# Kernel tuning notes

Hardware: AMD Instinct MI355X
Metric: run time of the kernel (lower is better)

Reference implementation:

```python
import jax, jax.numpy as jnp
import numpy as np

EPS = 1e-5

def layer_norm(x, gamma, beta):
    mu = jnp.mean(x, axis=-1, keepdims=True)
    var = jnp.mean(jnp.square(x - mu), axis=-1, keepdims=True)
    return (x - mu) * jax.lax.rsqrt(var + EPS) * gamma + beta

def setup_inputs() -> dict:
    key = jax.random.key(0)
    ks = jax.random.split(key, 8)
    B, N, CZ, C = 1, 512, 128, 128
    s_z = 1.0 / np.sqrt(CZ)
    s_c = 1.0 / np.sqrt(C)
    return {
        "pair_rep": jax.random.normal(ks[0], (B, N, N, CZ), dtype=jnp.float32),
        "ln1_gamma": jnp.ones((CZ,), jnp.float32),
        "ln1_beta": jnp.zeros((CZ,), jnp.float32),
        "w_gate_a": jax.random.normal(ks[1], (CZ, C), jnp.float32) * s_z,
        "w_gate_b": jax.random.normal(ks[2], (CZ, C), jnp.float32) * s_z,
        "w_a": jax.random.normal(ks[3], (CZ, C), jnp.float32) * s_z,
        "w_b": jax.random.normal(ks[4], (CZ, C), jnp.float32) * s_z,
        "ln2_gamma": jnp.ones((C,), jnp.float32),
        "ln2_beta": jnp.zeros((C,), jnp.float32),
        "w_out": jax.random.normal(ks[5], (C, CZ), jnp.float32) * s_c,
        "w_gate": jax.random.normal(ks[6], (CZ, CZ), jnp.float32) * s_z,
    }

def reference(pair_rep, ln1_gamma, ln1_beta, w_gate_a, w_gate_b, w_a, w_b,
              ln2_gamma, ln2_beta, w_out, w_gate):
    # pair_rep: [B, N, N, CZ]
    z = layer_norm(pair_rep, ln1_gamma, ln1_beta)
    a = jax.nn.sigmoid(z @ w_gate_a) * (z @ w_a)   # [B, N, N, C]
    b = jax.nn.sigmoid(z @ w_gate_b) * (z @ w_b)   # [B, N, N, C]
    g = jax.nn.sigmoid(z @ w_gate)                 # [B, N, N, CZ]
    # triangle multiplicative update (outgoing): sum over third node k
    upd = jnp.einsum('bikc,bjkc->bijc', a, b)      # [B, N, N, C]
    upd = layer_norm(upd, ln2_gamma, ln2_beta) @ w_out  # [B, N, N, CZ]
    return g * upd
```

## Files before the change

kernel.cpp:

```cpp
#include <hip/hip_runtime.h>

#define N_ 512
#define NPOS (N_*N_)
#define CD 128

typedef unsigned short ushort_t;
typedef unsigned int   uint_t;
typedef __bf16 bf16_t;
typedef bf16_t  bf16x8 __attribute__((ext_vector_type(8)));
typedef float   f32x4  __attribute__((ext_vector_type(4)));
typedef unsigned short u16x4 __attribute__((ext_vector_type(4)));
typedef uint_t  u32x4 __attribute__((ext_vector_type(4)));

__device__ __forceinline__ float bf2f(ushort_t h) {
  union { uint_t u; float f; } v; v.u = ((uint_t)h) << 16; return v.f;
}
__device__ __forceinline__ ushort_t f2bf(float f) {
  union { float f; uint_t u; } v; v.f = f;
  uint_t u = v.u;
  return (ushort_t)((u + 0x7FFFu + ((u >> 16) & 1u)) >> 16);
}
__device__ __forceinline__ float sigm(float x) { return 1.0f / (1.0f + __expf(-x)); }

__global__ void k_tw(const float* s0, const float* s1, const float* s2,
                     const float* s3, const float* s4, const float* s5,
                     ushort_t* dst) {
  const float* s;
  switch (blockIdx.x) {
    case 0: s = s0; break; case 1: s = s1; break; case 2: s = s2; break;
    case 3: s = s3; break; case 4: s = s4; break; default: s = s5; break;
  }
  ushort_t* d = dst + blockIdx.x * CD * CD;
  for (int idx = threadIdx.x; idx < CD * CD; idx += 256) {
    int c = idx >> 7, k = idx & 127;
    d[idx] = f2bf(s[k * CD + c]);
  }
}

__global__ void k_ln1(const float* __restrict__ x, const float* __restrict__ gma,
                      const float* __restrict__ bta, ushort_t* __restrict__ z) {
  const int tid  = threadIdx.x;
  const int l15  = tid & 15;
  const int row  = blockIdx.x * 16 + (tid >> 4);
  const float4* src = (const float4*)(x + (size_t)row * CD + l15 * 8);
  float4 v0 = src[0], v1 = src[1];
  float s = ((v0.x + v0.y) + (v0.z + v0.w)) + ((v1.x + v1.y) + (v1.z + v1.w));
  float q = ((v0.x*v0.x + v0.y*v0.y) + (v0.z*v0.z + v0.w*v0.w))
          + ((v1.x*v1.x + v1.y*v1.y) + (v1.z*v1.z + v1.w*v1.w));
  #pragma unroll
  for (int o = 1; o < 16; o <<= 1) { s += __shfl_xor(s, o, 64); q += __shfl_xor(q, o, 64); }
  float mu = s * (1.0f / 128.0f);
  float rs = rsqrtf(q * (1.0f / 128.0f) - mu * mu + 1e-5f);
  const float4* gp = (const float4*)(gma + l15 * 8);
  const float4* bp = (const float4*)(bta + l15 * 8);
  float4 g0 = gp[0], g1v = gp[1], b0 = bp[0], b1v = bp[1];
  uint_t w0 = (uint_t)f2bf((v0.x-mu)*rs*g0.x +b0.x ) | ((uint_t)f2bf((v0.y-mu)*rs*g0.y +b0.y ) << 16);
  uint_t w1 = (uint_t)f2bf((v0.z-mu)*rs*g0.z +b0.z ) | ((uint_t)f2bf((v0.w-mu)*rs*g0.w +b0.w ) << 16);
  uint_t w2 = (uint_t)f2bf((v1.x-mu)*rs*g1v.x+b1v.x) | ((uint_t)f2bf((v1.y-mu)*rs*g1v.y+b1v.y) << 16);
  uint_t w3 = (uint_t)f2bf((v1.z-mu)*rs*g1v.z+b1v.z) | ((uint_t)f2bf((v1.w-mu)*rs*g1v.w+b1v.w) << 16);
  u32x4 pk = {w0, w1, w2, w3};
  *(u32x4*)(z + (size_t)row * CD + l15 * 8) = pk;
}

__global__ __launch_bounds__(256, 1)
void k_proj(const ushort_t* __restrict__ z, const ushort_t* __restrict__ wT,
            ushort_t* __restrict__ aT, ushort_t* __restrict__ bT) {
  __shared__ ushort_t zl[128 * 128];
  __shared__ ushort_t tb[128][136];
  const int tid = threadIdx.x;
  const int lane = tid & 63, w = tid >> 6;
  const int qd = lane >> 4, l15 = lane & 15;

  bf16x8 wf[4][2][4];
  #pragma unroll
  for (int m = 0; m < 4; ++m)
    #pragma unroll
    for (int i = 0; i < 2; ++i)
      #pragma unroll
      for (int kk = 0; kk < 4; ++kk)
        wf[m][i][kk] = *(const bf16x8*)(wT + m * CD * CD + (w * 32 + i * 16 + l15) * CD + kk * 32 + qd * 8);

  const int TILES = 4;
  const int base = blockIdx.x * TILES;

  u32x4 st[8];
  {
    const u32x4* src = (const u32x4*)(z + (size_t)base * 128 * CD);
    #pragma unroll
    for (int i = 0; i < 8; ++i) st[i] = src[tid + i * 256];
  }

  for (int t = 0; t < TILES; ++t) {
    const int pos0 = (base + t) * 128;
    __syncthreads();
    {
      u32x4* dst = (u32x4*)zl;
      #pragma unroll
      for (int i = 0; i < 8; ++i) {
        int u = tid + i * 256, row = u >> 4;
        dst[(u & ~15) | ((u & 15) ^ (row & 7))] = st[i];
      }
    }
    __syncthreads();
    if (t + 1 < TILES) {
      const u32x4* src = (const u32x4*)(z + (size_t)(base + t + 1) * 128 * CD);
      #pragma unroll
      for (int i = 0; i < 8; ++i) st[i] = src[tid + i * 256];
    }

    #pragma unroll
    for (int ab = 0; ab < 2; ++ab) {
      f32x4 ag[2][8] = {}; f32x4 av[2][8] = {};
      #pragma unroll
      for (int kk = 0; kk < 4; ++kk) {
        bf16x8 zf[8];
        #pragma unroll
        for (int j = 0; j < 8; ++j) {
          int row = j * 16 + l15, kq = kk * 4 + qd;
          zf[j] = ((const bf16x8*)zl)[(row << 4) | (kq ^ (row & 7))];
        }
        #pragma unroll
        for (int j = 0; j < 8; ++j)
          #pragma unroll
          for (int i = 0; i < 2; ++i) {
            ag[i][j] = __builtin_amdgcn_mfma_f32_16x16x32_bf16(wf[ab * 2][i][kk],     zf[j], ag[i][j], 0, 0, 0);
            av[i][j] = __builtin_amdgcn_mfma_f32_16x16x32_bf16(wf[ab * 2 + 1][i][kk], zf[j], av[i][j], 0, 0, 0);
          }
      }
      #pragma unroll
      for (int i = 0; i < 2; ++i)
        #pragma unroll
        for (int j = 0; j < 8; ++j)
          #pragma unroll
          for (int r = 0; r < 4; ++r)
            tb[w * 32 + i * 16 + qd * 4 + r][j * 16 + l15] = f2bf(sigm(ag[i][j][r]) * av[i][j][r]);
      __syncthreads();
      {
        ushort_t* dst = ab ? bT : aT;
        #pragma unroll
        for (int it = 0; it < 8; ++it) {
          int idx = tid + it * 256;
          int row = idx >> 4, c16 = idx & 15;
          u32x4 v = *(const u32x4*)&tb[row][c16 * 8];
          *(u32x4*)&dst[(size_t)row * NPOS + pos0 + c16 * 8] = v;
        }
      }
      __syncthreads();
    }
  }
}

__device__ __forceinline__ int uofs(int row, int c4) {
  return (row * 4 + (c4 ^ ((row >> 1) & 3))) * 8;
}
__global__ void k_tri(const ushort_t* __restrict__ aT, const ushort_t* __restrict__ bT,
                      ushort_t* __restrict__ uT) {
  __shared__ u32x4 smem4[2176];
  ushort_t* lds = (ushort_t*)smem4;
  const int tid = threadIdx.x;
  const int lane = tid & 63, wid = tid >> 6;
  const int qd = lane >> 4, l15 = lane & 15;
  const int wm = wid & 1, wn = wid >> 1;
  const int c  = blockIdx.z;
  const int m0 = blockIdx.y * 128, n0 = blockIdx.x * 128;
  const ushort_t* A = aT + (size_t)c * NPOS;
  const ushort_t* B = bT + (size_t)c * NPOS;
  const int sr = tid >> 2, c4 = tid & 3;

  u32x4 rA0, rA1, rB0, rB1;
  rA0 = *(const u32x4*)&A[(size_t)(m0 + sr)      * N_ + c4 * 8];
  rA1 = *(const u32x4*)&A[(size_t)(m0 + 64 + sr) * N_ + c4 * 8];
  rB0 = *(const u32x4*)&B[(size_t)(n0 + sr)      * N_ + c4 * 8];
  rB1 = *(const u32x4*)&B[(size_t)(n0 + 64 + sr) * N_ + c4 * 8];
  *(u32x4*)&lds[       uofs(sr,      c4)] = rA0;
  *(u32x4*)&lds[       uofs(sr + 64, c4)] = rA1;
  *(u32x4*)&lds[8192 + uofs(sr,      c4)] = rB0;
  *(u32x4*)&lds[8192 + uofs(sr + 64, c4)] = rB1;

  f32x4 acc[4][4] = {};
  for (int it = 1; it <= 16; ++it) {
    __syncthreads();
    const int curb = (it - 1) & 1, nxt = it & 1;
    if (it < 16) {
      const int ko = it * 32;
      rA0 = *(const u32x4*)&A[(size_t)(m0 + sr)      * N_ + ko + c4 * 8];
      rA1 = *(const u32x4*)&A[(size_t)(m0 + 64 + sr) * N_ + ko + c4 * 8];
      rB0 = *(const u32x4*)&B[(size_t)(n0 + sr)      * N_ + ko + c4 * 8];
      rB1 = *(const u32x4*)&B[(size_t)(n0 + 64 + sr) * N_ + ko + c4 * 8];
    }
    const ushort_t* la = lds + curb * 4096;
    const ushort_t* lb = lds + 8192 + curb * 4096;
    bf16x8 af[4], bfr[4];
    #pragma unroll
    for (int t = 0; t < 4; ++t) af[t]  = *(const bf16x8*)&la[uofs(wm * 64 + t * 16 + l15, qd)];
    #pragma unroll
    for (int t = 0; t < 4; ++t) bfr[t] = *(const bf16x8*)&lb[uofs(wn * 64 + t * 16 + l15, qd)];
    #pragma unroll
    for (int i = 0; i < 4; ++i)
      #pragma unroll
      for (int j = 0; j < 4; ++j)
        acc[i][j] = __builtin_amdgcn_mfma_f32_16x16x32_bf16(af[i], bfr[j], acc[i][j], 0, 0, 0);
    if (it < 16) {
      *(u32x4*)&lds[nxt * 4096 +        uofs(sr,      c4)] = rA0;
      *(u32x4*)&lds[nxt * 4096 +        uofs(sr + 64, c4)] = rA1;
      *(u32x4*)&lds[8192 + nxt * 4096 + uofs(sr,      c4)] = rB0;
      *(u32x4*)&lds[8192 + nxt * 4096 + uofs(sr + 64, c4)] = rB1;
    }
  }
  __syncthreads();
  ushort_t (*tb)[136] = (ushort_t(*)[136])smem4;
  #pragma unroll
  for (int i = 0; i < 4; ++i)
    #pragma unroll
    for (int j = 0; j < 4; ++j)
      #pragma unroll
      for (int r2 = 0; r2 < 4; ++r2)
        tb[wm * 64 + i * 16 + qd * 4 + r2][wn * 64 + j * 16 + l15] = f2bf(acc[i][j][r2]);
  __syncthreads();
  ushort_t* U = uT + (size_t)c * NPOS;
  #pragma unroll
  for (int it = 0; it < 8; ++it) {
    int idx = tid + it * 256;
    int row = idx >> 4, c16 = idx & 15;
    u32x4 v = *(const u32x4*)&tb[row][c16 * 8];
    *(u32x4*)&U[(size_t)(m0 + row) * N_ + n0 + c16 * 8] = v;
  }
}

__global__ __launch_bounds__(256, 2)
void k_out(const ushort_t* __restrict__ uT, const ushort_t* __restrict__ wT,
           const float* __restrict__ pair,
           const float* __restrict__ g1, const float* __restrict__ b1,
           const float* __restrict__ g2, const float* __restrict__ b2,
           float* __restrict__ gout) {
  __shared__ ushort_t nu[128][136];
  __shared__ ushort_t zn[128][136];
  __shared__ float ps[2][128], pq[2][128];
  __shared__ float mu[128], rsd[128], gam[128], bet[128];
  const int tid = threadIdx.x;
  const int lane = tid & 63, wid = tid >> 6;
  const int qd = lane >> 4, l15 = lane & 15;
  const int pos0 = blockIdx.x * 128;
  const ushort_t* WgT = wT + 4 * CD * CD;
  const ushort_t* WoT = wT + 5 * CD * CD;

  if (tid < 128) { gam[tid] = g2[tid]; bet[tid] = b2[tid]; }

  {
    int r = tid >> 1, h = tid & 1;
    const float4* src = (const float4*)(pair + (size_t)(pos0 + r) * CD + h * 64);
    float s = 0.f, sq = 0.f;
    #pragma unroll
    for (int u = 0; u < 16; ++u) {
      float4 v = src[u];
      s  += (v.x + v.y) + (v.z + v.w);
      sq += (v.x*v.x + v.y*v.y) + (v.z*v.z + v.w*v.w);
    }
    ps[h][r] = s; pq[h][r] = sq;
  }
  __syncthreads();
  if (tid < 128) {
    float s = ps[0][tid] + ps[1][tid];
    float m = s * (1.0f / 128.0f);
    float v = (pq[0][tid] + pq[1][tid]) * (1.0f / 128.0f) - m * m;
    mu[tid] = m; rsd[tid] = rsqrtf(v + 1e-5f);
  }
  __syncthreads();
  {
    int r = tid >> 1, h = tid & 1;
    float m = mu[r], rs = rsd[r];
    const float4* src = (const float4*)(pair + (size_t)(pos0 + r) * CD + h * 64);
    const float4* gp = (const float4*)(g1 + h * 64);
    const float4* bp = (const float4*)(b1 + h * 64);
    #pragma unroll
    for (int u2 = 0; u2 < 8; ++u2) {
      float4 v0 = src[u2*2], v1 = src[u2*2+1];
      float4 ga = gp[u2*2], gb2 = gp[u2*2+1];
      float4 ba = bp[u2*2], bb2 = bp[u2*2+1];
      uint_t w0 = (uint_t)f2bf((v0.x-m)*rs*ga.x +ba.x ) | ((uint_t)f2bf((v0.y-m)*rs*ga.y +ba.y ) << 16);
      uint_t w1 = (uint_t)f2bf((v0.z-m)*rs*ga.z +ba.z ) | ((uint_t)f2bf((v0.w-m)*rs*ga.w +ba.w ) << 16);
      uint_t w2 = (uint_t)f2bf((v1.x-m)*rs*gb2.x+bb2.x) | ((uint_t)f2bf((v1.y-m)*rs*gb2.y+bb2.y) << 16);
      uint_t w3 = (uint_t)f2bf((v1.z-m)*rs*gb2.z+bb2.z) | ((uint_t)f2bf((v1.w-m)*rs*gb2.w+bb2.w) << 16);
      u32x4 pk = {w0, w1, w2, w3};
      *(u32x4*)&zn[r][h * 64 + u2 * 8] = pk;
    }
  }
  __syncthreads();

  {
    int p = tid & 127, h = tid >> 7;
    float s = 0.f, sq = 0.f;
    for (int cc = h * 64; cc < h * 64 + 64; ++cc) {
      ushort_t raw = uT[(size_t)cc * NPOS + pos0 + p];
      nu[p][cc] = raw;
      float v = bf2f(raw); s += v; sq += v * v;
    }
    ps[h][p] = s; pq[h][p] = sq;
  }
  __syncthreads();
  if (tid < 128) {
    float s = ps[0][tid] + ps[1][tid];
    float m = s * (1.0f / 128.0f);
    float v = (pq[0][tid] + pq[1][tid]) * (1.0f / 128.0f) - m * m;
    mu[tid] = m; rsd[tid] = rsqrtf(v + 1e-5f);
  }
  __syncthreads();
  {
    int p = tid & 127, h = tid >> 7;
    float m = mu[p], rs = rsd[p];
    for (int cc = h * 64; cc < h * 64 + 64; ++cc)
      nu[p][cc] = f2bf((bf2f(nu[p][cc]) - m) * rs * gam[cc] + bet[cc]);
  }
  __syncthreads();

  const int wm = wid & 1, wn = wid >> 1;
  f32x4 ao[4][4] = {}; f32x4 agt[4][4] = {};
  for (int kk = 0; kk < 4; ++kk) {
    bf16x8 afo[4], afg[4];
    #pragma unroll
    for (int i = 0; i < 4; ++i) {
      int wrow = (wm * 64 + i * 16 + l15) * CD + kk * 32 + qd * 8;
      afo[i] = *(const bf16x8*)(WoT + wrow);
      afg[i] = *(const bf16x8*)(WgT + wrow);
    }
    #pragma unroll
    for (int j = 0; j < 4; ++j) {
      bf16x8 bn = *(const bf16x8*)&nu[wn * 64 + j * 16 + l15][kk * 32 + qd * 8];
      bf16x8 bz = *(const bf16x8*)&zn[wn * 64 + j * 16 + l15][kk * 32 + qd * 8];
      #pragma unroll
      for (int i = 0; i < 4; ++i) {
        ao[i][j]  = __builtin_amdgcn_mfma_f32_16x16x32_bf16(afo[i], bn, ao[i][j],  0, 0, 0);
        agt[i][j] = __builtin_amdgcn_mfma_f32_16x16x32_bf16(afg[i], bz, agt[i][j], 0, 0, 0);
      }
    }
  }
  #pragma unroll
  for (int i = 0; i < 4; ++i) {
    int cz = wm * 64 + i * 16 + qd * 4;
    #pragma unroll
    for (int j = 0; j < 4; ++j) {
      int pos = pos0 + wn * 64 + j * 16 + l15;
      float4 pk;
      pk.x = sigm(agt[i][j][0]) * ao[i][j][0];
      pk.y = sigm(agt[i][j][1]) * ao[i][j][1];
      pk.z = sigm(agt[i][j][2]) * ao[i][j][2];
      pk.w = sigm(agt[i][j][3]) * ao[i][j][3];
      *(float4*)&gout[(size_t)pos * CD + cz] = pk;
    }
  }
}

extern "C" void kernel_launch(void* const* d_in, const int* in_sizes, int n_in,
                              void* d_out, int out_size, void* d_ws, size_t ws_size,
                              hipStream_t stream) {
  const float* pair = (const float*)d_in[0];
  const float* g1   = (const float*)d_in[1];
  const float* b1   = (const float*)d_in[2];
  const float* wga  = (const float*)d_in[3];
  const float* wgb  = (const float*)d_in[4];
  const float* wa   = (const float*)d_in[5];
  const float* wb   = (const float*)d_in[6];
  const float* g2   = (const float*)d_in[7];
  const float* b2   = (const float*)d_in[8];
  const float* wout = (const float*)d_in[9];
  const float* wg   = (const float*)d_in[10];

  char* ws = (char*)d_ws;
  ushort_t* z  = (ushort_t*)(ws);
  ushort_t* aT = (ushort_t*)(ws + 67108864);
  ushort_t* bT = (ushort_t*)(ws + 134217728);
  ushort_t* wT = (ushort_t*)(ws + 201326592);
  ushort_t* uT = z;
  float*    gb = (float*)d_out;

  k_tw  <<<6, 256, 0, stream>>>(wga, wa, wgb, wb, wg, wout, wT);
  k_ln1 <<<NPOS / 16, 256, 0, stream>>>(pair, g1, b1, z);
  k_proj<<<512, 256, 0, stream>>>(z, wT, aT, bT);
  k_tri <<<dim3(4, 4, 128), 256, 0, stream>>>(aT, bT, uT);
  k_out <<<2048, 256, 0, stream>>>(uT, wT, pair, g1, b1, g2, b2, gb);
}
```

Measured before the change: 547.0 us.

## Move gate projection into k_proj and fold LN2 affine into output weights

```diff
diff --git a/kernel.cpp b/kernel.cpp
--- a/kernel.cpp
+++ b/kernel.cpp
@@ -15,6 +15,12 @@
 __device__ __forceinline__ float bf2f(ushort_t h) {
   union { uint_t u; float f; } v; v.u = ((uint_t)h) << 16; return v.f;
 }
+__device__ __forceinline__ float bf2f_lo(uint_t w) {
+  union { uint_t u; float f; } v; v.u = w << 16; return v.f;
+}
+__device__ __forceinline__ float bf2f_hi(uint_t w) {
+  union { uint_t u; float f; } v; v.u = w & 0xffff0000u; return v.f;
+}
 __device__ __forceinline__ ushort_t f2bf(float f) {
   union { float f; uint_t u; } v; v.f = f;
   uint_t u = v.u;
@@ -24,16 +30,32 @@
 
 __global__ void k_tw(const float* s0, const float* s1, const float* s2,
                      const float* s3, const float* s4, const float* s5,
-                     ushort_t* dst) {
+                     ushort_t* dst, const float* lg2, const float* lb2, float* K12) {
   const float* s;
   switch (blockIdx.x) {
     case 0: s = s0; break; case 1: s = s1; break; case 2: s = s2; break;
     case 3: s = s3; break; case 4: s = s4; break; default: s = s5; break;
   }
   ushort_t* d = dst + blockIdx.x * CD * CD;
-  for (int idx = threadIdx.x; idx < CD * CD; idx += 256) {
-    int c = idx >> 7, k = idx & 127;
-    d[idx] = f2bf(s[k * CD + c]);
+  if (blockIdx.x == 5) {
+    for (int idx = threadIdx.x; idx < CD * CD; idx += 256) {
+      int cz = idx >> 7, ci = idx & 127;
+      d[idx] = f2bf(s[ci * CD + cz] * lg2[ci]);
+    }
+    if (threadIdx.x < 128) {
+      int cz = threadIdx.x;
+      float k1 = 0.f, k2 = 0.f;
+      for (int ci = 0; ci < 128; ++ci) {
+        float w = s[ci * CD + cz];
+        k1 += lg2[ci] * w; k2 += lb2[ci] * w;
+      }
+      K12[cz] = k1; K12[128 + cz] = k2;
+    }
+  } else {
+    for (int idx = threadIdx.x; idx < CD * CD; idx += 256) {
+      int c = idx >> 7, k = idx & 127;
+      d[idx] = f2bf(s[k * CD + c]);
+    }
   }
 }
 
@@ -64,16 +86,17 @@
 
 __global__ __launch_bounds__(256, 1)
 void k_proj(const ushort_t* __restrict__ z, const ushort_t* __restrict__ wT,
-            ushort_t* __restrict__ aT, ushort_t* __restrict__ bT) {
+            ushort_t* __restrict__ aT, ushort_t* __restrict__ bT,
+            float* __restrict__ g) {
   __shared__ ushort_t zl[128 * 128];
   __shared__ ushort_t tb[128][136];
   const int tid = threadIdx.x;
   const int lane = tid & 63, w = tid >> 6;
   const int qd = lane >> 4, l15 = lane & 15;
 
-  bf16x8 wf[4][2][4];
-  #pragma unroll
-  for (int m = 0; m < 4; ++m)
+  bf16x8 wf[5][2][4];
+  #pragma unroll
+  for (int m = 0; m < 5; ++m)
     #pragma unroll
     for (int i = 0; i < 2; ++i)
       #pragma unroll
@@ -146,6 +169,36 @@
         }
       }
       __syncthreads();
+    }
+
+    {
+      f32x4 acc[2][8] = {};
+      #pragma unroll
+      for (int kk = 0; kk < 4; ++kk) {
+        bf16x8 zf[8];
+        #pragma unroll
+        for (int j = 0; j < 8; ++j) {
+          int row = j * 16 + l15, kq = kk * 4 + qd;
+          zf[j] = ((const bf16x8*)zl)[(row << 4) | (kq ^ (row & 7))];
+        }
+        #pragma unroll
+        for (int j = 0; j < 8; ++j)
+          #pragma unroll
+          for (int i = 0; i < 2; ++i)
+            acc[i][j] = __builtin_amdgcn_mfma_f32_16x16x32_bf16(wf[4][i][kk], zf[j], acc[i][j], 0, 0, 0);
+      }
+      #pragma unroll
+      for (int i = 0; i < 2; ++i) {
+        int cz = w * 32 + i * 16 + qd * 4;
+        #pragma unroll
+        for (int j = 0; j < 8; ++j) {
+          int pos = pos0 + j * 16 + l15;
+          float4 pk;
+          pk.x = sigm(acc[i][j][0]); pk.y = sigm(acc[i][j][1]);
+          pk.z = sigm(acc[i][j][2]); pk.w = sigm(acc[i][j][3]);
+          *(float4*)&g[(size_t)pos * CD + cz] = pk;
+        }
+      }
     }
   }
 }
@@ -227,124 +280,105 @@
   }
 }
 
+__device__ __forceinline__ int nuofs(int row, int c16) {
+  return (row * 17 + (c16 ^ ((row >> 3) & 7))) * 8;
+}
 __global__ __launch_bounds__(256, 2)
 void k_out(const ushort_t* __restrict__ uT, const ushort_t* __restrict__ wT,
-           const float* __restrict__ pair,
-           const float* __restrict__ g1, const float* __restrict__ b1,
-           const float* __restrict__ g2, const float* __restrict__ b2,
-           float* __restrict__ gout) {
-  __shared__ ushort_t nu[128][136];
-  __shared__ ushort_t zn[128][136];
-  __shared__ float ps[2][128], pq[2][128];
-  __shared__ float mu[128], rsd[128], gam[128], bet[128];
+           const float* __restrict__ K12, float* gout) {
+  __shared__ ushort_t nu[128 * 17 * 8];
+  __shared__ float red[2][4][16][8];
+  __shared__ float muL[128], rsL[128], K1s[128], K2s[128];
   const int tid = threadIdx.x;
   const int lane = tid & 63, wid = tid >> 6;
   const int qd = lane >> 4, l15 = lane & 15;
   const int pos0 = blockIdx.x * 128;
-  const ushort_t* WgT = wT + 4 * CD * CD;
+  const int pch = tid & 15, cbase = tid >> 4;
   const ushort_t* WoT = wT + 5 * CD * CD;
 
-  if (tid < 128) { gam[tid] = g2[tid]; bet[tid] = b2[tid]; }
-
-  {
-    int r = tid >> 1, h = tid & 1;
-    const float4* src = (const float4*)(pair + (size_t)(pos0 + r) * CD + h * 64);
-    float s = 0.f, sq = 0.f;
-    #pragma unroll
-    for (int u = 0; u < 16; ++u) {
-      float4 v = src[u];
-      s  += (v.x + v.y) + (v.z + v.w);
-      sq += (v.x*v.x + v.y*v.y) + (v.z*v.z + v.w*v.w);
-    }
-    ps[h][r] = s; pq[h][r] = sq;
+  if (tid < 128) { K1s[tid] = K12[tid]; K2s[tid] = K12[128 + tid]; }
+
+  uint_t c8[8][4];
+  #pragma unroll
+  for (int i = 0; i < 8; ++i) {
+    u32x4 v = *(const u32x4*)&uT[(size_t)(cbase * 8 + i) * NPOS + pos0 + pch * 8];
+    c8[i][0] = v[0]; c8[i][1] = v[1]; c8[i][2] = v[2]; c8[i][3] = v[3];
+  }
+
+  float s8[8] = {}, q8[8] = {};
+  #pragma unroll
+  for (int i = 0; i < 8; ++i)
+    #pragma unroll
+    for (int wd = 0; wd < 4; ++wd) {
+      float vlo = bf2f_lo(c8[i][wd]), vhi = bf2f_hi(c8[i][wd]);
+      s8[wd * 2]     += vlo; q8[wd * 2]     += vlo * vlo;
+      s8[wd * 2 + 1] += vhi; q8[wd * 2 + 1] += vhi * vhi;
+    }
+  #pragma unroll
+  for (int r = 0; r < 8; ++r) {
+    s8[r] += __shfl_xor(s8[r], 16, 64); q8[r] += __shfl_xor(q8[r], 16, 64);
+    s8[r] += __shfl_xor(s8[r], 32, 64); q8[r] += __shfl_xor(q8[r], 32, 64);
+  }
+  if (lane < 16) {
+    #pragma unroll
+    for (int r = 0; r < 8; ++r) { red[0][wid][lane][r] = s8[r]; red[1][wid][lane][r] = q8[r]; }
+  }
+
+  #pragma unroll
+  for (int r = 0; r < 8; ++r) {
+    u32x4 t;
+    #pragma unroll
+    for (int k = 0; k < 4; ++k) {
+      uint_t a = c8[2 * k][r >> 1], b = c8[2 * k + 1][r >> 1];
+      uint_t sh = (r & 1) * 16;
+      t[k] = ((a >> sh) & 0xffffu) | (((b >> sh) & 0xffffu) << 16);
+    }
+    *(u32x4*)&nu[nuofs(pch * 8 + r, cbase)] = t;
   }
   __syncthreads();
+
   if (tid < 128) {
-    float s = ps[0][tid] + ps[1][tid];
+    int p2 = tid >> 3, r2 = tid & 7;
+    float s = red[0][0][p2][r2] + red[0][1][p2][r2] + red[0][2][p2][r2] + red[0][3][p2][r2];
+    float q = red[1][0][p2][r2] + red[1][1][p2][r2] + red[1][2][p2][r2] + red[1][3][p2][r2];
     float m = s * (1.0f / 128.0f);
-    float v = (pq[0][tid] + pq[1][tid]) * (1.0f / 128.0f) - m * m;
-    mu[tid] = m; rsd[tid] = rsqrtf(v + 1e-5f);
+    float v = q * (1.0f / 128.0f) - m * m;
+    muL[tid] = m; rsL[tid] = rsqrtf(v + 1e-5f);
   }
   __syncthreads();
-  {
-    int r = tid >> 1, h = tid & 1;
-    float m = mu[r], rs = rsd[r];
-    const float4* src = (const float4*)(pair + (size_t)(pos0 + r) * CD + h * 64);
-    const float4* gp = (const float4*)(g1 + h * 64);
-    const float4* bp = (const float4*)(b1 + h * 64);
-    #pragma unroll
-    for (int u2 = 0; u2 < 8; ++u2) {
-      float4 v0 = src[u2*2], v1 = src[u2*2+1];
-      float4 ga = gp[u2*2], gb2 = gp[u2*2+1];
-      float4 ba = bp[u2*2], bb2 = bp[u2*2+1];
-      uint_t w0 = (uint_t)f2bf((v0.x-m)*rs*ga.x +ba.x ) | ((uint_t)f2bf((v0.y-m)*rs*ga.y +ba.y ) << 16);
-      uint_t w1 = (uint_t)f2bf((v0.z-m)*rs*ga.z +ba.z ) | ((uint_t)f2bf((v0.w-m)*rs*ga.w +ba.w ) << 16);
-      uint_t w2 = (uint_t)f2bf((v1.x-m)*rs*gb2.x+bb2.x) | ((uint_t)f2bf((v1.y-m)*rs*gb2.y+bb2.y) << 16);
-      uint_t w3 = (uint_t)f2bf((v1.z-m)*rs*gb2.z+bb2.z) | ((uint_t)f2bf((v1.w-m)*rs*gb2.w+bb2.w) << 16);
-      u32x4 pk = {w0, w1, w2, w3};
-      *(u32x4*)&zn[r][h * 64 + u2 * 8] = pk;
-    }
-  }
-  __syncthreads();
-
-  {
-    int p = tid & 127, h = tid >> 7;
-    float s = 0.f, sq = 0.f;
-    for (int cc = h * 64; cc < h * 64 + 64; ++cc) {
-      ushort_t raw = uT[(size_t)cc * NPOS + pos0 + p];
-      nu[p][cc] = raw;
-      float v = bf2f(raw); s += v; sq += v * v;
-    }
-    ps[h][p] = s; pq[h][p] = sq;
-  }
-  __syncthreads();
-  if (tid < 128) {
-    float s = ps[0][tid] + ps[1][tid];
-    float m = s * (1.0f / 128.0f);
-    float v = (pq[0][tid] + pq[1][tid]) * (1.0f / 128.0f) - m * m;
-    mu[tid] = m; rsd[tid] = rsqrtf(v + 1e-5f);
-  }
-  __syncthreads();
-  {
-    int p = tid & 127, h = tid >> 7;
-    float m = mu[p], rs = rsd[p];
-    for (int cc = h * 64; cc < h * 64 + 64; ++cc)
-      nu[p][cc] = f2bf((bf2f(nu[p][cc]) - m) * rs * gam[cc] + bet[cc]);
-  }
-  __syncthreads();
 
   const int wm = wid & 1, wn = wid >> 1;
-  f32x4 ao[4][4] = {}; f32x4 agt[4][4] = {};
+  f32x4 acc[4][4] = {};
   for (int kk = 0; kk < 4; ++kk) {
-    bf16x8 afo[4], afg[4];
-    #pragma unroll
-    for (int i = 0; i < 4; ++i) {
-      int wrow = (wm * 64 + i * 16 + l15) * CD + kk * 32 + qd * 8;
-      afo[i] = *(const bf16x8*)(WoT + wrow);
-      afg[i] = *(const bf16x8*)(WgT + wrow);
-    }
+    bf16x8 afo[4];
+    #pragma unroll
+    for (int i = 0; i < 4; ++i)
+      afo[i] = *(const bf16x8*)(WoT + (wm * 64 + i * 16 + l15) * CD + kk * 32 + qd * 8);
     #pragma unroll
     for (int j = 0; j < 4; ++j) {
-      bf16x8 bn = *(const bf16x8*)&nu[wn * 64 + j * 16 + l15][kk * 32 + qd * 8];
-      bf16x8 bz = *(const bf16x8*)&zn[wn * 64 + j * 16 + l15][kk * 32 + qd * 8];
-      #pragma unroll
-      for (int i = 0; i < 4; ++i) {
-        ao[i][j]  = __builtin_amdgcn_mfma_f32_16x16x32_bf16(afo[i], bn, ao[i][j],  0, 0, 0);
-        agt[i][j] = __builtin_amdgcn_mfma_f32_16x16x32_bf16(afg[i], bz, agt[i][j], 0, 0, 0);
-      }
-    }
-  }
+      bf16x8 bn = *(const bf16x8*)&nu[nuofs(wn * 64 + j * 16 + l15, kk * 4 + qd)];
+      #pragma unroll
+      for (int i = 0; i < 4; ++i)
+        acc[i][j] = __builtin_amdgcn_mfma_f32_16x16x32_bf16(afo[i], bn, acc[i][j], 0, 0, 0);
+    }
+  }
+
   #pragma unroll
   for (int i = 0; i < 4; ++i) {
     int cz = wm * 64 + i * 16 + qd * 4;
+    float4 k1 = *(const float4*)&K1s[cz];
+    float4 k2 = *(const float4*)&K2s[cz];
     #pragma unroll
     for (int j = 0; j < 4; ++j) {
-      int pos = pos0 + wn * 64 + j * 16 + l15;
+      int pl = wn * 64 + j * 16 + l15;
+      float m = muL[pl], rr = rsL[pl];
+      int pos = pos0 + pl;
+      float4 gv = *(const float4*)&gout[(size_t)pos * CD + cz];
       float4 pk;
-      pk.x = sigm(agt[i][j][0]) * ao[i][j][0];
-      pk.y = sigm(agt[i][j][1]) * ao[i][j][1];
-      pk.z = sigm(agt[i][j][2]) * ao[i][j][2];
-      pk.w = sigm(agt[i][j][3]) * ao[i][j][3];
+      pk.x = gv.x * (rr * (acc[i][j][0] - m * k1.x) + k2.x);
+      pk.y = gv.y * (rr * (acc[i][j][1] - m * k1.y) + k2.y);
+      pk.z = gv.z * (rr * (acc[i][j][2] - m * k1.z) + k2.z);
+      pk.w = gv.w * (rr * (acc[i][j][3] - m * k1.w) + k2.w);
       *(float4*)&gout[(size_t)pos * CD + cz] = pk;
     }
   }
@@ -366,16 +400,17 @@
   const float* wg   = (const float*)d_in[10];
 
   char* ws = (char*)d_ws;
-  ushort_t* z  = (ushort_t*)(ws);
-  ushort_t* aT = (ushort_t*)(ws + 67108864);
-  ushort_t* bT = (ushort_t*)(ws + 134217728);
-  ushort_t* wT = (ushort_t*)(ws + 201326592);
+  ushort_t* z   = (ushort_t*)(ws);
+  ushort_t* aT  = (ushort_t*)(ws + 67108864);
+  ushort_t* bT  = (ushort_t*)(ws + 134217728);
+  ushort_t* wT  = (ushort_t*)(ws + 201326592);
+  float*    K12 = (float*)(ws + 201326592 + 196608);
   ushort_t* uT = z;
   float*    gb = (float*)d_out;
 
-  k_tw  <<<6, 256, 0, stream>>>(wga, wa, wgb, wb, wg, wout, wT);
+  k_tw  <<<6, 256, 0, stream>>>(wga, wa, wgb, wb, wg, wout, wT, g2, b2, K12);
   k_ln1 <<<NPOS / 16, 256, 0, stream>>>(pair, g1, b1, z);
-  k_proj<<<512, 256, 0, stream>>>(z, wT, aT, bT);
+  k_proj<<<512, 256, 0, stream>>>(z, wT, aT, bT, gb);
   k_tri <<<dim3(4, 4, 128), 256, 0, stream>>>(aT, bT, uT);
-  k_out <<<2048, 256, 0, stream>>>(uT, wT, pair, g1, b1, g2, b2, gb);
-}
+  k_out <<<2048, 256, 0, stream>>>(uT, wT, K12, gb);
+}
```

New measurement: 544.0 us. Within noise of the previous version (-0.6%).
